# Performance work log

Measured on AMD Instinct MI355X. Metric: run time of the kernel, lower is better.

## Reference

```python
import jax, jax.numpy as jnp
import numpy as np

N_TARGETS = 6
RADIUS = 2
RECLEN = 2 * RADIUS + 1  # 5
SWAP_RC = True


def setup_inputs() -> dict:
    key = jax.random.key(0)
    heatmap = jax.random.uniform(key, (128, 1, 512, 512), dtype=jnp.float32)
    return {"heatmap": heatmap}


def _sample_one(hm):
    # hm: [H, W]. Iteratively: avg-pool (VALID), take first (row-major) argmax
    # of the pooled map, zero the corresponding RECLEN x RECLEN window, repeat.
    H, W = hm.shape
    pw = W - RECLEN + 1  # pooled width

    def step(hm, _):
        # sum-pool == avg-pool up to a positive constant -> same argmax
        agg = jax.lax.reduce_window(
            hm, 0.0, jax.lax.add,
            window_dimensions=(RECLEN, RECLEN),
            window_strides=(1, 1), padding='VALID')
        idx = jnp.argmax(agg)  # first occurrence, row-major (matches torch nonzero()[0])
        r = idx // pw
        c = idx % pw
        # suppress the window in the ORIGINAL heatmap (pooled index i -> window [i, i+RECLEN))
        hm = jax.lax.dynamic_update_slice(
            hm, jnp.zeros((RECLEN, RECLEN), hm.dtype), (r, c))
        return hm, jnp.stack([r + RADIUS, c + RADIUS])

    _, coords = jax.lax.scan(step, hm, None, length=N_TARGETS)
    return coords  # [N_TARGETS, 2] int


def reference(heatmap):
    # heatmap: [B, 1, H, W]
    coords = jax.vmap(_sample_one)(heatmap[:, 0])  # [B, N_TARGETS, 2] as (row, col)
    if SWAP_RC:
        coords = coords[:, :, ::-1]  # (col, row)
    return coords
```

## Files before the change

kernel.cpp:

```cpp
#include <hip/hip_runtime.h>
#include <hip/hip_bf16.h>

#define HM_W 512
#define HM_H 512
#define PW   508

__device__ __forceinline__ void load_row8(const float* __restrict__ hm, int y, int c0, float v[8]) {
    const float4* rp = reinterpret_cast<const float4*>(hm + y * HM_W + c0);
    float4 a = rp[0];
    float4 b = rp[1];
    v[0]=a.x; v[1]=a.y; v[2]=a.z; v[3]=a.w;
    v[4]=b.x; v[5]=b.y; v[6]=b.z; v[7]=b.w;
}

__device__ __forceinline__ void row_best_shfl(const float s[8], int lane, float& bv, int& bc) {
    float cb[12];
#pragma unroll
    for (int j = 0; j < 8; ++j) cb[j] = s[j];
#pragma unroll
    for (int j = 0; j < 4; ++j) cb[8 + j] = __shfl_down(s[j], 1);
    bv = -__builtin_inff();
    bc = 0x7fffffff;
    int c0 = lane * 8;
#pragma unroll
    for (int j = 0; j < 8; ++j) {
        int c = c0 + j;
        float w = cb[j] + cb[j + 1] + cb[j + 2] + cb[j + 3] + cb[j + 4];
        if (c < PW && w > bv) { bv = w; bc = c; }
    }
#pragma unroll
    for (int m = 1; m < 64; m <<= 1) {
        float ov = __shfl_xor(bv, m);
        int   oc = __shfl_xor(bc, m);
        if (ov > bv || (ov == bv && oc < bc)) { bv = ov; bc = oc; }
    }
}

__global__ void phase1_kernel(const float* __restrict__ hm_all,
                              float* __restrict__ rowv_ws, int* __restrict__ rowc_ws) {
    int b = blockIdx.y;
    int wave = threadIdx.x >> 6;
    int lane = threadIdx.x & 63;
    int c0 = lane * 8;
    const float* hm = hm_all + (size_t)b * HM_W * HM_H;

    int rbase = (blockIdx.x * 4 + wave) * 16;
    if (rbase >= PW) return;

    float w0[8], w1[8], w2[8], w3[8], w4[8];
    load_row8(hm, rbase + 0, c0, w0);
    load_row8(hm, rbase + 1, c0, w1);
    load_row8(hm, rbase + 2, c0, w2);
    load_row8(hm, rbase + 3, c0, w3);

#pragma unroll
    for (int rr = 0; rr < 16; ++rr) {
        int y = rbase + rr;
        if (y >= PW) break;
        load_row8(hm, y + 4, c0, w4);
        float s[8];
#pragma unroll
        for (int j = 0; j < 8; ++j)
            s[j] = ((((w0[j] + w1[j]) + w2[j]) + w3[j]) + w4[j]);
        float bv; int bc;
        row_best_shfl(s, lane, bv, bc);
        if (lane == 0) {
            rowv_ws[b * 512 + y] = bv;
            rowc_ws[b * 512 + y] = bc;
        }
#pragma unroll
        for (int j = 0; j < 8; ++j) { w0[j] = w1[j]; w1[j] = w2[j]; w2[j] = w3[j]; w3[j] = w4[j]; }
    }
}

__global__ void __launch_bounds__(640) phase2_kernel(const float* __restrict__ hm_all,
                              const float* __restrict__ rowv_ws,
                              const int* __restrict__ rowc_ws,
                              int* __restrict__ out) {
    int b = blockIdx.x;
    const float* hm = hm_all + (size_t)b * HM_W * HM_H;
    int t = threadIdx.x;
    int wave = t >> 6, lane = t & 63;
    int c0 = lane * 8;

    __shared__ float rowv[512];
    __shared__ int   rowc[512];
    __shared__ float updv[2][9];
    __shared__ int   updc[2][9];
    __shared__ float obv[2];
    __shared__ int   obr[2], obc[2];

    if (t < 512) {
        if (t < PW) { rowv[t] = rowv_ws[b * 512 + t]; rowc[t] = rowc_ws[b * 512 + t]; }
        else        { rowv[t] = -__builtin_inff();    rowc[t] = 0; }
    }
    __syncthreads();

    int zrr[6], zcc[6];
    int pz0 = 0, pzn = 0;
    int fr, fc;

    {
        float bv = -__builtin_inff(); int bi = 0x7fffffff;
#pragma unroll
        for (int j = 0; j < 8; ++j) {
            int idx = j * 64 + lane;
            float v = rowv[idx];
            if (v > bv) { bv = v; bi = idx; }
        }
#pragma unroll
        for (int m = 1; m < 64; m <<= 1) {
            float ov = __shfl_xor(bv, m);
            int   oi = __shfl_xor(bi, m);
            if (ov > bv || (ov == bv && oi < bi)) { bv = ov; bi = oi; }
        }
        fr = bi; fc = rowc[fr];
    }
    zrr[0] = fr; zcc[0] = fc;
    if (t == 0) {
        out[b * 12 + 0] = fc + 2;
        out[b * 12 + 1] = fr + 2;
    }

#pragma unroll
    for (int it = 0; it < 5; ++it) {
        int wbuf = it & 1;
        int rbuf = wbuf ^ 1;

        int zlo = fr - 4 < 0 ? 0 : fr - 4;
        int zhi = fr + 4 > PW - 1 ? PW - 1 : fr + 4;
        int zn  = zhi - zlo + 1;

        if (t < 9 && t < pzn) {
            rowv[pz0 + t] = updv[rbuf][t];
            rowc[pz0 + t] = updc[rbuf][t];
        }

        if (wave < 9) {
            if (wave < zn) {
                int y = zlo + wave;
                float s[8];
#pragma unroll
                for (int j = 0; j < 8; ++j) s[j] = 0.f;
#pragma unroll
                for (int i = 0; i < 5; ++i) {
                    float v[8];
                    load_row8(hm, y + i, c0, v);
#pragma unroll
                    for (int k = 0; k < 6; ++k) {
                        if (k <= it) {
                            if ((unsigned)(y + i - zrr[k]) < 5u) {
#pragma unroll
                                for (int j = 0; j < 8; ++j)
                                    if ((unsigned)(c0 + j - zcc[k]) < 5u) v[j] = 0.f;
                            }
                        }
                    }
#pragma unroll
                    for (int j = 0; j < 8; ++j) s[j] += v[j];
                }
                float nv; int nc;
                row_best_shfl(s, lane, nv, nc);
                if (lane == 0) { updv[wbuf][wave] = nv; updc[wbuf][wave] = nc; }
            }
        } else {
            float bv = -__builtin_inff(); int bi = 0x7fffffff;
#pragma unroll
            for (int j = 0; j < 8; ++j) {
                int idx = j * 64 + lane;
                float v = rowv[idx];
                unsigned u = (unsigned)(idx - pz0);
                if (u < (unsigned)pzn) v = updv[rbuf][u];
                if ((unsigned)(idx - zlo) < (unsigned)zn) v = -__builtin_inff();
                if (v > bv) { bv = v; bi = idx; }
            }
#pragma unroll
            for (int m = 1; m < 64; m <<= 1) {
                float ov = __shfl_xor(bv, m);
                int   oi = __shfl_xor(bi, m);
                if (ov > bv || (ov == bv && oi < bi)) { bv = ov; bi = oi; }
            }
            if (lane == 0) {
                int bc2 = rowc[bi];
                unsigned u = (unsigned)(bi - pz0);
                if (u < (unsigned)pzn) bc2 = updc[rbuf][u];
                obv[wbuf] = bv; obr[wbuf] = bi; obc[wbuf] = bc2;
            }
        }

        __syncthreads();

        {
            float bv = obv[wbuf]; int br = obr[wbuf]; int bc2 = obc[wbuf];
#pragma unroll
            for (int u = 0; u < 9; ++u) {
                if (u < zn) {
                    int yy = zlo + u;
                    float v = updv[wbuf][u];
                    if (v > bv || (v == bv && yy < br)) { bv = v; br = yy; bc2 = updc[wbuf][u]; }
                }
            }
            fr = br; fc = bc2;
        }
        zrr[it + 1] = fr; zcc[it + 1] = fc;
        if (t == 0) {
            out[b * 12 + (it + 1) * 2 + 0] = fc + 2;
            out[b * 12 + (it + 1) * 2 + 1] = fr + 2;
        }

        pz0 = zlo; pzn = zn;
    }
}

extern "C" void kernel_launch(void* const* d_in, const int* in_sizes, int n_in,
                              void* d_out, int out_size, void* d_ws, size_t ws_size,
                              hipStream_t stream) {
    const float* hm = (const float*)d_in[0];
    int* out = (int*)d_out;
    float* rowv_ws = (float*)d_ws;
    int*   rowc_ws = (int*)((char*)d_ws + (size_t)128 * 512 * sizeof(float));

    phase1_kernel<<<dim3(8, 128), dim3(256), 0, stream>>>(hm, rowv_ws, rowc_ws);
    phase2_kernel<<<dim3(128), dim3(640), 0, stream>>>(hm, rowv_ws, rowc_ws, out);
}
```

Before: 50.89 us.

## Fuse row-pooling and iterative suppression kernels using a last-block atomic counter

Merges the two launches into one kernel. Eight blocks per image each compute per-row pooled maxima, and an atomic counter per image picks the last block to finish, which then runs the six-step suppression loop. The suppression loop is reshaped onto 4 waves: three waves each recompute up to three rows and the fourth does the global argmax. This removes a kernel launch boundary and lets the tail overlap across images, at the cost of an added memset, an atomic, less parallelism in the recompute, and reliance on acquire/release visibility of workspace writes.

```diff
diff --git a/kernel.cpp b/kernel.cpp
--- a/kernel.cpp
+++ b/kernel.cpp
@@ -4,6 +4,7 @@
 #define HM_W 512
 #define HM_H 512
 #define PW   508
+#define NBATCH 128
 
 __device__ __forceinline__ void load_row8(const float* __restrict__ hm, int y, int c0, float v[8]) {
     const float4* rp = reinterpret_cast<const float4*>(hm + y * HM_W + c0);
@@ -36,52 +37,15 @@
     }
 }
 
-__global__ void phase1_kernel(const float* __restrict__ hm_all,
-                              float* __restrict__ rowv_ws, int* __restrict__ rowc_ws) {
-    int b = blockIdx.y;
-    int wave = threadIdx.x >> 6;
-    int lane = threadIdx.x & 63;
-    int c0 = lane * 8;
-    const float* hm = hm_all + (size_t)b * HM_W * HM_H;
-
-    int rbase = (blockIdx.x * 4 + wave) * 16;
-    if (rbase >= PW) return;
-
-    float w0[8], w1[8], w2[8], w3[8], w4[8];
-    load_row8(hm, rbase + 0, c0, w0);
-    load_row8(hm, rbase + 1, c0, w1);
-    load_row8(hm, rbase + 2, c0, w2);
-    load_row8(hm, rbase + 3, c0, w3);
-
-#pragma unroll
-    for (int rr = 0; rr < 16; ++rr) {
-        int y = rbase + rr;
-        if (y >= PW) break;
-        load_row8(hm, y + 4, c0, w4);
-        float s[8];
-#pragma unroll
-        for (int j = 0; j < 8; ++j)
-            s[j] = ((((w0[j] + w1[j]) + w2[j]) + w3[j]) + w4[j]);
-        float bv; int bc;
-        row_best_shfl(s, lane, bv, bc);
-        if (lane == 0) {
-            rowv_ws[b * 512 + y] = bv;
-            rowc_ws[b * 512 + y] = bc;
-        }
-#pragma unroll
-        for (int j = 0; j < 8; ++j) { w0[j] = w1[j]; w1[j] = w2[j]; w2[j] = w3[j]; w3[j] = w4[j]; }
-    }
-}
-
-__global__ void __launch_bounds__(640) phase2_kernel(const float* __restrict__ hm_all,
-                              const float* __restrict__ rowv_ws,
-                              const int* __restrict__ rowc_ws,
-                              int* __restrict__ out) {
-    int b = blockIdx.x;
-    const float* hm = hm_all + (size_t)b * HM_W * HM_H;
+__global__ void __launch_bounds__(256) fused_kernel(const float* __restrict__ hm_all,
+                              float* __restrict__ rowv_ws, int* __restrict__ rowc_ws,
+                              int* __restrict__ cnt, int* __restrict__ out) {
     int t = threadIdx.x;
     int wave = t >> 6, lane = t & 63;
     int c0 = lane * 8;
+    int blk = blockIdx.x;
+    int b = blk >> 3;
+    const float* hm = hm_all + (size_t)b * HM_W * HM_H;
 
     __shared__ float rowv[512];
     __shared__ int   rowc[512];
@@ -89,10 +53,48 @@
     __shared__ int   updc[2][9];
     __shared__ float obv[2];
     __shared__ int   obr[2], obc[2];
-
-    if (t < 512) {
-        if (t < PW) { rowv[t] = rowv_ws[b * 512 + t]; rowc[t] = rowc_ws[b * 512 + t]; }
-        else        { rowv[t] = -__builtin_inff();    rowc[t] = 0; }
+    __shared__ int   lastFlag;
+
+    {
+        int rbase = ((blk & 7) * 4 + wave) * 16;
+        float w0[8], w1[8], w2[8], w3[8], w4[8];
+        load_row8(hm, rbase + 0, c0, w0);
+        load_row8(hm, rbase + 1, c0, w1);
+        load_row8(hm, rbase + 2, c0, w2);
+        load_row8(hm, rbase + 3, c0, w3);
+
+#pragma unroll
+        for (int rr = 0; rr < 16; ++rr) {
+            int y = rbase + rr;
+            if (y >= PW) break;
+            load_row8(hm, y + 4, c0, w4);
+            float s[8];
+#pragma unroll
+            for (int j = 0; j < 8; ++j)
+                s[j] = ((((w0[j] + w1[j]) + w2[j]) + w3[j]) + w4[j]);
+            float bv; int bc;
+            row_best_shfl(s, lane, bv, bc);
+            if (lane == 0) {
+                rowv_ws[b * 512 + y] = bv;
+                rowc_ws[b * 512 + y] = bc;
+            }
+#pragma unroll
+            for (int j = 0; j < 8; ++j) { w0[j] = w1[j]; w1[j] = w2[j]; w2[j] = w3[j]; w3[j] = w4[j]; }
+        }
+    }
+
+    __syncthreads();
+    if (t == 0) {
+        int old = __hip_atomic_fetch_add(&cnt[b], 1, __ATOMIC_ACQ_REL,
+                                         __HIP_MEMORY_SCOPE_AGENT);
+        lastFlag = (old == 7);
+    }
+    __syncthreads();
+    if (!lastFlag) return;
+
+    for (int i = t; i < 512; i += 256) {
+        if (i < PW) { rowv[i] = rowv_ws[b * 512 + i]; rowc[i] = rowc_ws[b * 512 + i]; }
+        else        { rowv[i] = -__builtin_inff();    rowc[i] = 0; }
     }
     __syncthreads();
 
@@ -136,34 +138,38 @@
             rowc[pz0 + t] = updc[rbuf][t];
         }
 
-        if (wave < 9) {
-            if (wave < zn) {
-                int y = zlo + wave;
-                float s[8];
-#pragma unroll
-                for (int j = 0; j < 8; ++j) s[j] = 0.f;
-#pragma unroll
-                for (int i = 0; i < 5; ++i) {
-                    float v[8];
-                    load_row8(hm, y + i, c0, v);
-#pragma unroll
-                    for (int k = 0; k < 6; ++k) {
-                        if (k <= it) {
-                            if ((unsigned)(y + i - zrr[k]) < 5u) {
-#pragma unroll
-                                for (int j = 0; j < 8; ++j)
-                                    if ((unsigned)(c0 + j - zcc[k]) < 5u) v[j] = 0.f;
+        if (wave < 3) {
+#pragma unroll
+            for (int q = 0; q < 3; ++q) {
+                int li = wave * 3 + q;
+                if (li < zn) {
+                    int y = zlo + li;
+                    float s[8];
+#pragma unroll
+                    for (int j = 0; j < 8; ++j) s[j] = 0.f;
+#pragma unroll
+                    for (int i = 0; i < 5; ++i) {
+                        float v[8];
+                        load_row8(hm, y + i, c0, v);
+#pragma unroll
+                        for (int k = 0; k < 6; ++k) {
+                            if (k <= it) {
+                                if ((unsigned)(y + i - zrr[k]) < 5u) {
+#pragma unroll
+                                    for (int j = 0; j < 8; ++j)
+                                        if ((unsigned)(c0 + j - zcc[k]) < 5u) v[j] = 0.f;
+                                }
                             }
                         }
+#pragma unroll
+                        for (int j = 0; j < 8; ++j) s[j] += v[j];
                     }
-#pragma unroll
-                    for (int j = 0; j < 8; ++j) s[j] += v[j];
+                    float nv; int nc;
+                    row_best_shfl(s, lane, nv, nc);
+                    if (lane == 0) { updv[wbuf][li] = nv; updc[wbuf][li] = nc; }
                 }
-                float nv; int nc;
-                row_best_shfl(s, lane, nv, nc);
-                if (lane == 0) { updv[wbuf][wave] = nv; updc[wbuf][wave] = nc; }
-            }
-        } else {
+            }
+        } else if (wave == 3) {
             float bv = -__builtin_inff(); int bi = 0x7fffffff;
 #pragma unroll
             for (int j = 0; j < 8; ++j) {
@@ -219,7 +225,8 @@
     int* out = (int*)d_out;
     float* rowv_ws = (float*)d_ws;
     int*   rowc_ws = (int*)((char*)d_ws + (size_t)128 * 512 * sizeof(float));
-
-    phase1_kernel<<<dim3(8, 128), dim3(256), 0, stream>>>(hm, rowv_ws, rowc_ws);
-    phase2_kernel<<<dim3(128), dim3(640), 0, stream>>>(hm, rowv_ws, rowc_ws, out);
-}
+    int*   cnt     = (int*)((char*)d_ws + (size_t)2 * 128 * 512 * sizeof(float));
+
+    hipMemsetAsync(cnt, 0, NBATCH * sizeof(int), stream);
+    fused_kernel<<<dim3(1024), dim3(256), 0, stream>>>(hm, rowv_ws, rowc_ws, cnt, out);
+}
```

Measured after the change: 109.6 us. +115.3%, slower.
